# Kernel tuning notes

Measured on AMD Instinct MI355X. Metric: run time of the kernel, lower is better.

The kernel has to match this reference:

```python
import jax, jax.numpy as jnp
import numpy as np

NB_X = 32
NB_Y = 32
EPS = 1e-08


def setup_inputs() -> dict:
    key = jax.random.key(0)
    ks = jax.random.split(key, 10)
    B, L, F, H, D = 16, NB_X * NB_Y + 1, 768, 12, 64
    s = 0.02
    return {
        'x': jax.random.normal(ks[0], (B, L, F), dtype=jnp.float32),
        'wq': jax.random.normal(ks[1], (F, H, D), dtype=jnp.float32) * s,
        'bq': jnp.zeros((H, D), dtype=jnp.float32),
        'wk': jax.random.normal(ks[2], (F, H, D), dtype=jnp.float32) * s,
        'bk': jnp.zeros((H, D), dtype=jnp.float32),
        'wv': jax.random.normal(ks[3], (F, H, D), dtype=jnp.float32) * s,
        'bv': jnp.zeros((H, D), dtype=jnp.float32),
        'wo': jax.random.normal(ks[4], (H, D, F), dtype=jnp.float32) * s,
        'bo': jnp.zeros((F,), dtype=jnp.float32),
        'toeplitz_params': jax.random.normal(ks[5], (H, 4 * NB_X * NB_Y), dtype=jnp.float32),
    }


def _dist_index():
    # relative-position index over the 2D patch grid, flattened to (L0*L0,)
    gi = np.arange(NB_X)
    gj = np.arange(NB_Y)
    idx = ((gi[:, None, None, None] - gi[None, None, :, None] + NB_X) * 2 * NB_Y
           + gj[None, :, None, None] - gj[None, None, None, :] + NB_Y)
    return jnp.asarray(idx.reshape(-1), dtype=jnp.int32)


def reference(x, wq, bq, wk, bk, wv, bv, wo, bo, toeplitz_params):
    H, D = wq.shape[1], wq.shape[2]
    L0 = NB_X * NB_Y  # number of patch tokens (seq len = L0 + 1 with CLS)

    q = jnp.einsum('bqf,fhd->bqhd', x, wq) + bq
    k = jnp.einsum('bkf,fhd->bkhd', x, wk) + bk
    v = jnp.einsum('bkf,fhd->bkhd', x, wv) + bv

    # relu-kernelized scores
    q = jax.nn.relu(q / jnp.sqrt(jnp.float32(D))) + EPS
    k = jax.nn.relu(k) + EPS
    attn = jnp.einsum('bqhd,bkhd->bhqk', q, k)  # [B,H,L,L]

    # per-head Toeplitz relative-position mask via gather
    tm = jnp.take(toeplitz_params, _dist_index(), axis=1).reshape(H, L0, L0)
    tm = jnp.pad(tm, [[0, 0], [1, 0], [0, 0]], constant_values=1.0)
    tm = jnp.pad(tm, [[0, 0], [0, 0], [1, 0]], constant_values=1.0)

    attn = attn * jnp.abs(tm)[None] + EPS
    attn = attn / jnp.sum(attn, axis=-1, keepdims=True)  # sum-normalization

    out = jnp.einsum('bhqk,bkhd->bqhd', attn, v)
    return jnp.einsum('bqhd,hdf->bqf', out, wo) + bo
```

## Files before the change

kernel.cpp:

```cpp
#include <hip/hip_runtime.h>
#include <hip/hip_bf16.h>

#define BB 16
#define LQ 1025
#define FF 768
#define HH 12
#define DD 64
#define EPSF 1e-8f

#define TPSTRIDE 6400
#define QPART_CLS 6270
#define VSTRIDE 1040

typedef unsigned short u16;
typedef __attribute__((ext_vector_type(8))) short  bf16x8;
typedef __attribute__((ext_vector_type(4))) float  f32x4;

__device__ __forceinline__ float bf2f(u16 u) {
    union { unsigned int i; float f; } c;
    c.i = ((unsigned int)u) << 16;
    return c.f;
}

__device__ __forceinline__ u16 f2bf(float f) {
    union { float f; unsigned int i; } c;
    c.f = f;
    unsigned int x = c.i;
    unsigned int r = (x + 0x7fffu + ((x >> 16) & 1u)) >> 16;
    return (u16)r;
}

__global__ __launch_bounds__(256) void convert_x(
    const float* __restrict__ x, u16* __restrict__ xb, int n4)
{
    int i = blockIdx.x * blockDim.x + threadIdx.x;
    const int stride = gridDim.x * blockDim.x;
    for (; i < n4; i += stride) {
        float4 f = ((const float4*)x)[i];
        ushort4 o;
        o.x = f2bf(f.x); o.y = f2bf(f.y); o.z = f2bf(f.z); o.w = f2bf(f.w);
        ((ushort4*)xb)[i] = o;
    }
}

__global__ __launch_bounds__(256) void transpose_w(
    const float* __restrict__ wq, const float* __restrict__ wk,
    const float* __restrict__ wv, const float* __restrict__ wo,
    u16* __restrict__ wqt, u16* __restrict__ wkt,
    u16* __restrict__ wvt, u16* __restrict__ wot)
{
    const int z = blockIdx.z;
    const float* __restrict__ src = (z == 0) ? wq : (z == 1) ? wk : (z == 2) ? wv : wo;
    u16* __restrict__ dst         = (z == 0) ? wqt : (z == 1) ? wkt : (z == 2) ? wvt : wot;

    const int c0 = blockIdx.x * 64;
    const int r0 = blockIdx.y * 64;

    __shared__ u16 tile[64][72];

    const int t   = threadIdx.x;
    const int row = t >> 2;
    const int cs  = (t & 3) << 4;

    {
        const float* p = src + (size_t)(r0 + row) * 768 + c0 + cs;
#pragma unroll
        for (int q = 0; q < 4; ++q) {
            float4 f = *(const float4*)(p + 4 * q);
            ushort4 o;
            o.x = f2bf(f.x); o.y = f2bf(f.y); o.z = f2bf(f.z); o.w = f2bf(f.w);
            *(ushort4*)&tile[row][cs + 4 * q] = o;
        }
    }
    __syncthreads();
    {
        u16* p = dst + (size_t)(c0 + row) * 768 + r0 + cs;
#pragma unroll
        for (int q = 0; q < 4; ++q) {
            ushort4 o;
            o.x = tile[cs + 4 * q + 0][row];
            o.y = tile[cs + 4 * q + 1][row];
            o.z = tile[cs + 4 * q + 2][row];
            o.w = tile[cs + 4 * q + 3][row];
            *(ushort4*)(p + 4 * q) = o;
        }
    }
}

__global__ __launch_bounds__(256) void build_tpa(
    const float* __restrict__ tp, float* __restrict__ tpa)
{
    int i = blockIdx.x * 256 + threadIdx.x;
    if (i >= HH * TPSTRIDE) return;
    int h = i / TPSTRIDE, j = i - h * TPSTRIDE;
    float v;
    if (j < 64) v = 0.f;
    else if (j < 64 + 4096) v = fabsf(tp[h * 4096 + (j - 64)]);
    else v = 1.f;
    tpa[i] = v;
}

__global__ __launch_bounds__(256) void transpose_v(
    const u16* __restrict__ vbuf, u16* __restrict__ vtbuf)
{
    const int bh = blockIdx.y;
    const int lt = blockIdx.x;
    __shared__ u16 tile[64][65];
    const int t   = threadIdx.x;
    const int row = t >> 2;
    const int seg = (t & 3) << 4;

    {
        int l = lt * 64 + row;
        if (l < LQ) {
            const ushort4* p = (const ushort4*)(vbuf + ((size_t)bh * LQ + l) * 64 + seg);
#pragma unroll
            for (int q = 0; q < 4; ++q) {
                ushort4 a = p[q];
                tile[row][seg + 4 * q + 0] = a.x;
                tile[row][seg + 4 * q + 1] = a.y;
                tile[row][seg + 4 * q + 2] = a.z;
                tile[row][seg + 4 * q + 3] = a.w;
            }
        } else {
#pragma unroll
            for (int j = 0; j < 16; ++j) tile[row][seg + j] = 0;
        }
    }
    __syncthreads();
    {
        int kbase = lt * 64 + seg;
        if (kbase + 16 <= VSTRIDE) {
            u16* q = vtbuf + (size_t)bh * 64 * VSTRIDE + (size_t)row * VSTRIDE + kbase;
#pragma unroll
            for (int g = 0; g < 4; ++g) {
                ushort4 o;
                o.x = tile[seg + 4 * g + 0][row];
                o.y = tile[seg + 4 * g + 1][row];
                o.z = tile[seg + 4 * g + 2][row];
                o.w = tile[seg + 4 * g + 3][row];
                *(ushort4*)(q + 4 * g) = o;
            }
        }
    }
}

__global__ __launch_bounds__(256) void gemm_qkv_mfma(
    const u16* __restrict__ xb,
    const u16* __restrict__ wqt, const u16* __restrict__ wkt,
    const u16* __restrict__ wvt,
    const float* __restrict__ bq, const float* __restrict__ bk,
    const float* __restrict__ bv,
    u16* __restrict__ qbuf, u16* __restrict__ kbuf, u16* __restrict__ vbuf)
{
    const int M  = BB * LQ;
    const int m0 = blockIdx.x * 128;
    const int h  = blockIdx.y;
    const int n0 = h * 64;

    __shared__ u16 As[128][40];
    __shared__ u16 Bq[64][40];
    __shared__ u16 Bk[64][40];
    __shared__ u16 Bv[64][40];

    const int t    = threadIdx.x;
    const int wave = t >> 6;
    const int lane = t & 63;
    const int quad = lane >> 4;
    const int l16  = lane & 15;

    const int sm   = t >> 1;
    const int sseg = (t & 1) << 4;
    const int bn   = t >> 2;
    const int bseg = (t & 3) << 3;

    f32x4 acc[3][2][4];
#pragma unroll
    for (int ty = 0; ty < 3; ++ty)
#pragma unroll
        for (int i = 0; i < 2; ++i)
#pragma unroll
            for (int j = 0; j < 4; ++j)
                acc[ty][i][j] = (f32x4){0.f, 0.f, 0.f, 0.f};

    for (int k0 = 0; k0 < 768; k0 += 32) {
        __syncthreads();
        {
            int gm = m0 + sm;
            if (gm < M) {
                const uint4* p = (const uint4*)(xb + (size_t)gm * 768 + k0 + sseg);
                *(uint4*)&As[sm][sseg]     = p[0];
                *(uint4*)&As[sm][sseg + 8] = p[1];
            } else {
                uint4 z; z.x = 0; z.y = 0; z.z = 0; z.w = 0;
                *(uint4*)&As[sm][sseg]     = z;
                *(uint4*)&As[sm][sseg + 8] = z;
            }
        }
        {
            size_t off = (size_t)(n0 + bn) * 768 + k0 + bseg;
            *(uint4*)&Bq[bn][bseg] = *(const uint4*)(wqt + off);
            *(uint4*)&Bk[bn][bseg] = *(const uint4*)(wkt + off);
            *(uint4*)&Bv[bn][bseg] = *(const uint4*)(wvt + off);
        }
        __syncthreads();

        bf16x8 af0 = *(const bf16x8*)&As[(wave << 5) + l16][quad * 8];
        bf16x8 af1 = *(const bf16x8*)&As[(wave << 5) + 16 + l16][quad * 8];
#pragma unroll
        for (int j = 0; j < 4; ++j) {
            bf16x8 bq8 = *(const bf16x8*)&Bq[16 * j + l16][quad * 8];
            acc[0][0][j] = __builtin_amdgcn_mfma_f32_16x16x32_bf16(af0, bq8, acc[0][0][j], 0, 0, 0);
            acc[0][1][j] = __builtin_amdgcn_mfma_f32_16x16x32_bf16(af1, bq8, acc[0][1][j], 0, 0, 0);
            bf16x8 bk8 = *(const bf16x8*)&Bk[16 * j + l16][quad * 8];
            acc[1][0][j] = __builtin_amdgcn_mfma_f32_16x16x32_bf16(af0, bk8, acc[1][0][j], 0, 0, 0);
            acc[1][1][j] = __builtin_amdgcn_mfma_f32_16x16x32_bf16(af1, bk8, acc[1][1][j], 0, 0, 0);
            bf16x8 bv8 = *(const bf16x8*)&Bv[16 * j + l16][quad * 8];
            acc[2][0][j] = __builtin_amdgcn_mfma_f32_16x16x32_bf16(af0, bv8, acc[2][0][j], 0, 0, 0);
            acc[2][1][j] = __builtin_amdgcn_mfma_f32_16x16x32_bf16(af1, bv8, acc[2][1][j], 0, 0, 0);
        }
    }

#pragma unroll
    for (int i = 0; i < 2; ++i) {
#pragma unroll
        for (int reg = 0; reg < 4; ++reg) {
            int gm = m0 + (wave << 5) + (i << 4) + quad * 4 + reg;
            if (gm >= M) continue;
            int b_idx = gm / LQ;
            int l     = gm - b_idx * LQ;
            size_t obase = ((size_t)(b_idx * HH + h) * LQ + l) * 64;
#pragma unroll
            for (int j = 0; j < 4; ++j) {
                int d = 16 * j + l16;
                float vq = acc[0][i][j][reg] + bq[n0 + d];
                vq = fmaxf(vq * 0.125f, 0.f) + EPSF;
                qbuf[obase + d] = f2bf(vq);
                float vk = acc[1][i][j][reg] + bk[n0 + d];
                vk = fmaxf(vk, 0.f) + EPSF;
                kbuf[obase + d] = f2bf(vk);
                float vv = acc[2][i][j][reg] + bv[n0 + d];
                vbuf[obase + d] = f2bf(vv);
            }
        }
    }
}

__global__ __launch_bounds__(256) void attn_fused(
    const u16* __restrict__ qbuf, const u16* __restrict__ kbuf,
    const u16* __restrict__ vtbuf, const float* __restrict__ tpa,
    u16* __restrict__ obuf)
{
    const int bh = blockIdx.y;
    const int b  = bh / HH;
    const int h  = bh - b * HH;
    const int q0 = blockIdx.x * 64;

    __shared__ u16 SQ[64][72];
    __shared__ u16 Ks[64][72];
    __shared__ u16 Vt[64][72];

    const int t    = threadIdx.x;
    const int wave = t >> 6;
    const int lane = t & 63;
    const int quad = lane >> 4;
    const int l16  = lane & 15;
    const int w16  = wave << 4;

    const size_t base  = (size_t)bh * LQ * 64;
    const size_t vbase = (size_t)bh * 64 * VSTRIDE;
    const float* tb = tpa + h * TPSTRIDE;

    const int srow = t >> 2;
    const int sseg = (t & 3) << 4;

    {
        const uint4* qp = (const uint4*)(qbuf + base + (size_t)(q0 + srow) * 64 + sseg);
        *(uint4*)&SQ[srow][sseg]     = qp[0];
        *(uint4*)&SQ[srow][sseg + 8] = qp[1];
    }

    const int qi = q0 + w16 + l16;
    int qpart;
    if (qi == 0) qpart = QPART_CLS;
    else { int qm1 = qi - 1; qpart = (((qm1 >> 5) + 32) << 6) + (qm1 & 31) + 32; }

    int idx[16];
#pragma unroll
    for (int ct = 0; ct < 4; ++ct)
#pragma unroll
        for (int reg = 0; reg < 4; ++reg) {
            int km1 = ct * 16 + quad * 4 + reg - 1;
            idx[ct * 4 + reg] = 64 + qpart - (((km1 >> 5) << 6) + (km1 & 31));
        }

    uint4 kr0, kr1, vr0, vr1;
    {
        uint4 z; z.x = 0; z.y = 0; z.z = 0; z.w = 0;
        int ki = srow;
        if (ki < LQ) {
            const uint4* kp = (const uint4*)(kbuf + base + (size_t)ki * 64 + sseg);
            kr0 = kp[0]; kr1 = kp[1];
        } else { kr0 = z; kr1 = z; }
        const uint4* vp = (const uint4*)(vtbuf + vbase + (size_t)srow * VSTRIDE + sseg);
        vr0 = vp[0]; vr1 = vp[1];
    }

    __syncthreads();

    bf16x8 qf0 = *(const bf16x8*)&SQ[w16 + l16][quad * 8];
    bf16x8 qf1 = *(const bf16x8*)&SQ[w16 + l16][32 + quad * 8];

    f32x4 acc_o[4];
#pragma unroll
    for (int dt = 0; dt < 4; ++dt) acc_o[dt] = (f32x4){0.f, 0.f, 0.f, 0.f};
    float den = 0.f;

    for (int kt = 0; kt < 17; ++kt) {
        __syncthreads();

        *(uint4*)&Ks[srow][sseg]     = kr0;
        *(uint4*)&Ks[srow][sseg + 8] = kr1;
        *(uint4*)&Vt[srow][sseg]     = vr0;
        *(uint4*)&Vt[srow][sseg + 8] = vr1;

        float tmv[16];
#pragma unroll
        for (int e = 0; e < 16; ++e) tmv[e] = tb[idx[e]];

        if (kt < 16) {
            uint4 z; z.x = 0; z.y = 0; z.z = 0; z.w = 0;
            int k0n = (kt + 1) * 64;
            int ki = k0n + srow;
            if (ki < LQ) {
                const uint4* kp = (const uint4*)(kbuf + base + (size_t)ki * 64 + sseg);
                kr0 = kp[0]; kr1 = kp[1];
            } else { kr0 = z; kr1 = z; }
            int vcol = k0n + sseg;
            if (vcol + 16 <= VSTRIDE) {
                const uint4* vp = (const uint4*)(vtbuf + vbase + (size_t)srow * VSTRIDE + vcol);
                vr0 = vp[0]; vr1 = vp[1];
            } else { vr0 = z; vr1 = z; }
        }

        __syncthreads();

        f32x4 acc_s[4];
#pragma unroll
        for (int ct = 0; ct < 4; ++ct) {
            bf16x8 kf0 = *(const bf16x8*)&Ks[ct * 16 + l16][quad * 8];
            bf16x8 kf1 = *(const bf16x8*)&Ks[ct * 16 + l16][32 + quad * 8];
            f32x4 z = (f32x4){0.f, 0.f, 0.f, 0.f};
            z = __builtin_amdgcn_mfma_f32_16x16x32_bf16(kf0, qf0, z, 0, 0, 0);
            z = __builtin_amdgcn_mfma_f32_16x16x32_bf16(kf1, qf1, z, 0, 0, 0);
            acc_s[ct] = z;
        }

        if (kt == 0) { if (quad == 0) tmv[0] = 1.0f; }

#pragma unroll
        for (int ct = 0; ct < 4; ++ct) {
            float s0 = acc_s[ct][0] * tmv[ct * 4 + 0] + EPSF;
            float s1 = acc_s[ct][1] * tmv[ct * 4 + 1] + EPSF;
            float s2 = acc_s[ct][2] * tmv[ct * 4 + 2] + EPSF;
            float s3 = acc_s[ct][3] * tmv[ct * 4 + 3] + EPSF;
            den += (s0 + s1) + (s2 + s3);
            ushort4 w;
            w.x = f2bf(s0); w.y = f2bf(s1); w.z = f2bf(s2); w.w = f2bf(s3);
            *(ushort4*)&SQ[w16 + l16][ct * 16 + quad * 4] = w;
        }
#pragma unroll
        for (int e = 0; e < 16; ++e) idx[e] -= 128;

        __syncthreads();

        {
            bf16x8 a0 = *(const bf16x8*)&SQ[w16 + l16][quad * 8];
            bf16x8 a1 = *(const bf16x8*)&SQ[w16 + l16][32 + quad * 8];
#pragma unroll
            for (int dt = 0; dt < 4; ++dt) {
                bf16x8 b0 = *(const bf16x8*)&Vt[dt * 16 + l16][quad * 8];
                bf16x8 b1 = *(const bf16x8*)&Vt[dt * 16 + l16][32 + quad * 8];
                acc_o[dt] = __builtin_amdgcn_mfma_f32_16x16x32_bf16(a0, b0, acc_o[dt], 0, 0, 0);
                acc_o[dt] = __builtin_amdgcn_mfma_f32_16x16x32_bf16(a1, b1, acc_o[dt], 0, 0, 0);
            }
        }
    }

    den += __shfl_xor(den, 16);
    den += __shfl_xor(den, 32);
    float invd = 1.f / den;

#pragma unroll
    for (int reg = 0; reg < 4; ++reg) {
        int r = quad * 4 + reg;
        float iv = __shfl(invd, r, 64);
        int qrow = q0 + w16 + r;
        if (qrow < LQ) {
            u16* p = obuf + ((size_t)(b * LQ + qrow) * HH + h) * 64;
#pragma unroll
            for (int dt = 0; dt < 4; ++dt)
                p[dt * 16 + l16] = f2bf(acc_o[dt][reg] * iv);
        }
    }
}

__global__ __launch_bounds__(256) void gemm_out_mfma(
    const u16* __restrict__ a, const u16* __restrict__ wot,
    const float* __restrict__ bo, float* __restrict__ out)
{
    const int M  = BB * LQ;
    const int m0 = blockIdx.x * 128;
    const int n0 = blockIdx.y * 64;

    __shared__ u16 As[128][40];
    __shared__ u16 Bs[64][40];

    const int t    = threadIdx.x;
    const int wave = t >> 6;
    const int lane = t & 63;
    const int quad = lane >> 4;
    const int l16  = lane & 15;

    const int sm   = t >> 1;
    const int sseg = (t & 1) << 4;
    const int bn   = t >> 2;
    const int bseg = (t & 3) << 3;

    f32x4 acc[2][4];
#pragma unroll
    for (int i = 0; i < 2; ++i)
#pragma unroll
        for (int j = 0; j < 4; ++j)
            acc[i][j] = (f32x4){0.f, 0.f, 0.f, 0.f};

    for (int k0 = 0; k0 < 768; k0 += 32) {
        __syncthreads();
        {
            int gm = m0 + sm;
            if (gm < M) {
                const uint4* p = (const uint4*)(a + (size_t)gm * 768 + k0 + sseg);
                *(uint4*)&As[sm][sseg]     = p[0];
                *(uint4*)&As[sm][sseg + 8] = p[1];
            } else {
                uint4 z; z.x = 0; z.y = 0; z.z = 0; z.w = 0;
                *(uint4*)&As[sm][sseg]     = z;
                *(uint4*)&As[sm][sseg + 8] = z;
            }
        }
        {
            *(uint4*)&Bs[bn][bseg] =
                *(const uint4*)(wot + (size_t)(n0 + bn) * 768 + k0 + bseg);
        }
        __syncthreads();

        bf16x8 af0 = *(const bf16x8*)&As[(wave << 5) + l16][quad * 8];
        bf16x8 af1 = *(const bf16x8*)&As[(wave << 5) + 16 + l16][quad * 8];
#pragma unroll
        for (int j = 0; j < 4; ++j) {
            bf16x8 b8 = *(const bf16x8*)&Bs[16 * j + l16][quad * 8];
            acc[0][j] = __builtin_amdgcn_mfma_f32_16x16x32_bf16(af0, b8, acc[0][j], 0, 0, 0);
            acc[1][j] = __builtin_amdgcn_mfma_f32_16x16x32_bf16(af1, b8, acc[1][j], 0, 0, 0);
        }
    }

#pragma unroll
    for (int i = 0; i < 2; ++i) {
#pragma unroll
        for (int reg = 0; reg < 4; ++reg) {
            int gm = m0 + (wave << 5) + (i << 4) + quad * 4 + reg;
            if (gm >= M) continue;
            float* p = out + (size_t)gm * 768;
#pragma unroll
            for (int j = 0; j < 4; ++j) {
                int n = n0 + 16 * j + l16;
                p[n] = acc[i][j][reg] + bo[n];
            }
        }
    }
}

extern "C" void kernel_launch(void* const* d_in, const int* in_sizes, int n_in,
                              void* d_out, int out_size, void* d_ws, size_t ws_size,
                              hipStream_t stream) {
    const float* x  = (const float*)d_in[0];
    const float* wq = (const float*)d_in[1];
    const float* bq = (const float*)d_in[2];
    const float* wk = (const float*)d_in[3];
    const float* bk = (const float*)d_in[4];
    const float* wv = (const float*)d_in[5];
    const float* bv = (const float*)d_in[6];
    const float* wo = (const float*)d_in[7];
    const float* bo = (const float*)d_in[8];
    const float* tp = (const float*)d_in[9];
    float* out = (float*)d_out;

    const size_t per = (size_t)BB * HH * LQ * DD;
    const size_t wsz = (size_t)FF * FF;
    u16* ws16  = (u16*)d_ws;
    u16* qbuf  = ws16;
    u16* kbuf  = qbuf + per;
    u16* vbuf  = kbuf + per;
    u16* xb    = vbuf + per;
    u16* wqt   = xb + per;
    u16* wkt   = wqt + wsz;
    u16* wvt   = wkt + wsz;
    u16* wot   = wvt + wsz;
    float* tpa = (float*)(wot + wsz);

    u16* vtbuf = xb;
    u16* obuf  = vbuf;

    convert_x<<<2048, 256, 0, stream>>>(x, xb, (int)(per / 4));
    dim3 gt(12, 12, 4);
    transpose_w<<<gt, 256, 0, stream>>>(wq, wk, wv, wo, wqt, wkt, wvt, wot);
    build_tpa<<<(HH * TPSTRIDE + 255) / 256, 256, 0, stream>>>(tp, tpa);

    dim3 g1(129, 12);
    gemm_qkv_mfma<<<g1, 256, 0, stream>>>(xb, wqt, wkt, wvt, bq, bk, bv,
                                          qbuf, kbuf, vbuf);

    dim3 gv(17, BB * HH);
    transpose_v<<<gv, 256, 0, stream>>>(vbuf, vtbuf);

    dim3 g2(17, BB * HH);
    attn_fused<<<g2, 256, 0, stream>>>(qbuf, kbuf, vtbuf, tpa, obuf);

    dim3 g3(129, 12);
    gemm_out_mfma<<<g3, 256, 0, stream>>>(obuf, wot, bo, out);
}
```

Measured before the change: 484.8 us.

## Use 128x128 wave tiles in both GEMMs and double-buffer K/V in attention

Both projection GEMMs now use a 128x128 block tile with a 2x2 wave layout, giving each wave a 64x64 sub-tile. For the QKV GEMM, the contiguous wqt/wkt/wvt buffers are treated as a single 2304-wide weight matrix, and a new kernel packs the three biases into one array. The attention kernel double-buffers its K and V shared-memory tiles and prefetches two tiles ahead, which cuts the per-iteration barriers from three to one. The intent is more MFMA work per shared-memory load and fewer synchronisations, at the cost of more registers, more LDS and fewer blocks in the grid.

```diff
diff --git a/kernel.cpp b/kernel.cpp
--- a/kernel.cpp
+++ b/kernel.cpp
@@ -100,6 +100,16 @@
     tpa[i] = v;
 }
 
+__global__ __launch_bounds__(256) void pack_bias(
+    const float* __restrict__ bq, const float* __restrict__ bk,
+    const float* __restrict__ bv, float* __restrict__ bias_cat)
+{
+    int i = blockIdx.x * 256 + threadIdx.x;
+    if (i >= 2304) return;
+    float v = (i < 768) ? bq[i] : (i < 1536) ? bk[i - 768] : bv[i - 1536];
+    bias_cat[i] = v;
+}
+
 __global__ __launch_bounds__(256) void transpose_v(
     const u16* __restrict__ vbuf, u16* __restrict__ vtbuf)
 {
@@ -146,42 +156,34 @@
 }
 
 __global__ __launch_bounds__(256) void gemm_qkv_mfma(
-    const u16* __restrict__ xb,
-    const u16* __restrict__ wqt, const u16* __restrict__ wkt,
-    const u16* __restrict__ wvt,
-    const float* __restrict__ bq, const float* __restrict__ bk,
-    const float* __restrict__ bv,
+    const u16* __restrict__ xb, const u16* __restrict__ wt,
+    const float* __restrict__ bias_cat,
     u16* __restrict__ qbuf, u16* __restrict__ kbuf, u16* __restrict__ vbuf)
 {
-    const int M  = BB * LQ;
-    const int m0 = blockIdx.x * 128;
-    const int h  = blockIdx.y;
-    const int n0 = h * 64;
+    const int M   = BB * LQ;
+    const int m0  = blockIdx.x * 128;
+    const int n0g = blockIdx.y * 128;
 
     __shared__ u16 As[128][40];
-    __shared__ u16 Bq[64][40];
-    __shared__ u16 Bk[64][40];
-    __shared__ u16 Bv[64][40];
+    __shared__ u16 Bs[128][40];
 
     const int t    = threadIdx.x;
     const int wave = t >> 6;
     const int lane = t & 63;
     const int quad = lane >> 4;
     const int l16  = lane & 15;
+    const int wm   = (wave >> 1) << 6;
+    const int wn   = (wave & 1) << 6;
 
     const int sm   = t >> 1;
     const int sseg = (t & 1) << 4;
-    const int bn   = t >> 2;
-    const int bseg = (t & 3) << 3;
-
-    f32x4 acc[3][2][4];
-#pragma unroll
-    for (int ty = 0; ty < 3; ++ty)
-#pragma unroll
-        for (int i = 0; i < 2; ++i)
-#pragma unroll
-            for (int j = 0; j < 4; ++j)
-                acc[ty][i][j] = (f32x4){0.f, 0.f, 0.f, 0.f};
+
+    f32x4 acc[4][4];
+#pragma unroll
+    for (int i = 0; i < 4; ++i)
+#pragma unroll
+        for (int j = 0; j < 4; ++j)
+            acc[i][j] = (f32x4){0.f, 0.f, 0.f, 0.f};
 
     for (int k0 = 0; k0 < 768; k0 += 32) {
         __syncthreads();
@@ -198,49 +200,44 @@
             }
         }
         {
-            size_t off = (size_t)(n0 + bn) * 768 + k0 + bseg;
-            *(uint4*)&Bq[bn][bseg] = *(const uint4*)(wqt + off);
-            *(uint4*)&Bk[bn][bseg] = *(const uint4*)(wkt + off);
-            *(uint4*)&Bv[bn][bseg] = *(const uint4*)(wvt + off);
+            const uint4* p = (const uint4*)(wt + (size_t)(n0g + sm) * 768 + k0 + sseg);
+            *(uint4*)&Bs[sm][sseg]     = p[0];
+            *(uint4*)&Bs[sm][sseg + 8] = p[1];
         }
         __syncthreads();
 
-        bf16x8 af0 = *(const bf16x8*)&As[(wave << 5) + l16][quad * 8];
-        bf16x8 af1 = *(const bf16x8*)&As[(wave << 5) + 16 + l16][quad * 8];
-#pragma unroll
-        for (int j = 0; j < 4; ++j) {
-            bf16x8 bq8 = *(const bf16x8*)&Bq[16 * j + l16][quad * 8];
-            acc[0][0][j] = __builtin_amdgcn_mfma_f32_16x16x32_bf16(af0, bq8, acc[0][0][j], 0, 0, 0);
-            acc[0][1][j] = __builtin_amdgcn_mfma_f32_16x16x32_bf16(af1, bq8, acc[0][1][j], 0, 0, 0);
-            bf16x8 bk8 = *(const bf16x8*)&Bk[16 * j + l16][quad * 8];
-            acc[1][0][j] = __builtin_amdgcn_mfma_f32_16x16x32_bf16(af0, bk8, acc[1][0][j], 0, 0, 0);
-            acc[1][1][j] = __builtin_amdgcn_mfma_f32_16x16x32_bf16(af1, bk8, acc[1][1][j], 0, 0, 0);
-            bf16x8 bv8 = *(const bf16x8*)&Bv[16 * j + l16][quad * 8];
-            acc[2][0][j] = __builtin_amdgcn_mfma_f32_16x16x32_bf16(af0, bv8, acc[2][0][j], 0, 0, 0);
-            acc[2][1][j] = __builtin_amdgcn_mfma_f32_16x16x32_bf16(af1, bv8, acc[2][1][j], 0, 0, 0);
-        }
-    }
-
-#pragma unroll
-    for (int i = 0; i < 2; ++i) {
+        bf16x8 af[4], bf[4];
+#pragma unroll
+        for (int i = 0; i < 4; ++i) af[i] = *(const bf16x8*)&As[wm + 16 * i + l16][quad * 8];
+#pragma unroll
+        for (int j = 0; j < 4; ++j) bf[j] = *(const bf16x8*)&Bs[wn + 16 * j + l16][quad * 8];
+#pragma unroll
+        for (int i = 0; i < 4; ++i)
+#pragma unroll
+            for (int j = 0; j < 4; ++j)
+                acc[i][j] = __builtin_amdgcn_mfma_f32_16x16x32_bf16(af[i], bf[j], acc[i][j], 0, 0, 0);
+    }
+
+    const int type = (n0g >= 1536) ? 2 : (n0g >= 768) ? 1 : 0;
+    u16* __restrict__ outb = (type == 0) ? qbuf : (type == 1) ? kbuf : vbuf;
+    const int nbase = n0g - type * 768;
+
+#pragma unroll
+    for (int i = 0; i < 4; ++i) {
 #pragma unroll
         for (int reg = 0; reg < 4; ++reg) {
-            int gm = m0 + (wave << 5) + (i << 4) + quad * 4 + reg;
+            int gm = m0 + wm + 16 * i + quad * 4 + reg;
             if (gm >= M) continue;
             int b_idx = gm / LQ;
             int l     = gm - b_idx * LQ;
-            size_t obase = ((size_t)(b_idx * HH + h) * LQ + l) * 64;
 #pragma unroll
             for (int j = 0; j < 4; ++j) {
-                int d = 16 * j + l16;
-                float vq = acc[0][i][j][reg] + bq[n0 + d];
-                vq = fmaxf(vq * 0.125f, 0.f) + EPSF;
-                qbuf[obase + d] = f2bf(vq);
-                float vk = acc[1][i][j][reg] + bk[n0 + d];
-                vk = fmaxf(vk, 0.f) + EPSF;
-                kbuf[obase + d] = f2bf(vk);
-                float vv = acc[2][i][j][reg] + bv[n0 + d];
-                vbuf[obase + d] = f2bf(vv);
+                int nloc = nbase + wn + 16 * j + l16;
+                int h = nloc >> 6, d = nloc & 63;
+                float v = acc[i][j][reg] + bias_cat[n0g + wn + 16 * j + l16];
+                if (type == 0) v = fmaxf(v * 0.125f, 0.f) + EPSF;
+                else if (type == 1) v = fmaxf(v, 0.f) + EPSF;
+                outb[((size_t)(b_idx * HH + h) * LQ + l) * 64 + d] = f2bf(v);
             }
         }
     }
@@ -257,8 +254,8 @@
     const int q0 = blockIdx.x * 64;
 
     __shared__ u16 SQ[64][72];
-    __shared__ u16 Ks[64][72];
-    __shared__ u16 Vt[64][72];
+    __shared__ u16 Ks[2][64][72];
+    __shared__ u16 Vt[2][64][72];
 
     const int t    = threadIdx.x;
     const int wave = t >> 6;
@@ -311,26 +308,42 @@
     bf16x8 qf0 = *(const bf16x8*)&SQ[w16 + l16][quad * 8];
     bf16x8 qf1 = *(const bf16x8*)&SQ[w16 + l16][32 + quad * 8];
 
+    *(uint4*)&Ks[0][srow][sseg]     = kr0;
+    *(uint4*)&Ks[0][srow][sseg + 8] = kr1;
+    *(uint4*)&Vt[0][srow][sseg]     = vr0;
+    *(uint4*)&Vt[0][srow][sseg + 8] = vr1;
+
+    {
+        uint4 z; z.x = 0; z.y = 0; z.z = 0; z.w = 0;
+        int ki = 64 + srow;
+        if (ki < LQ) {
+            const uint4* kp = (const uint4*)(kbuf + base + (size_t)ki * 64 + sseg);
+            kr0 = kp[0]; kr1 = kp[1];
+        } else { kr0 = z; kr1 = z; }
+        int vcol = 64 + sseg;
+        const uint4* vp = (const uint4*)(vtbuf + vbase + (size_t)srow * VSTRIDE + vcol);
+        vr0 = vp[0]; vr1 = vp[1];
+    }
+
     f32x4 acc_o[4];
 #pragma unroll
     for (int dt = 0; dt < 4; ++dt) acc_o[dt] = (f32x4){0.f, 0.f, 0.f, 0.f};
     float den = 0.f;
 
+    __syncthreads();
+
     for (int kt = 0; kt < 17; ++kt) {
-        __syncthreads();
-
-        *(uint4*)&Ks[srow][sseg]     = kr0;
-        *(uint4*)&Ks[srow][sseg + 8] = kr1;
-        *(uint4*)&Vt[srow][sseg]     = vr0;
-        *(uint4*)&Vt[srow][sseg + 8] = vr1;
-
-        float tmv[16];
-#pragma unroll
-        for (int e = 0; e < 16; ++e) tmv[e] = tb[idx[e]];
+        const int p = kt & 1;
 
         if (kt < 16) {
+            *(uint4*)&Ks[p ^ 1][srow][sseg]     = kr0;
+            *(uint4*)&Ks[p ^ 1][srow][sseg + 8] = kr1;
+            *(uint4*)&Vt[p ^ 1][srow][sseg]     = vr0;
+            *(uint4*)&Vt[p ^ 1][srow][sseg + 8] = vr1;
+        }
+        if (kt < 15) {
             uint4 z; z.x = 0; z.y = 0; z.z = 0; z.w = 0;
-            int k0n = (kt + 1) * 64;
+            int k0n = (kt + 2) * 64;
             int ki = k0n + srow;
             if (ki < LQ) {
                 const uint4* kp = (const uint4*)(kbuf + base + (size_t)ki * 64 + sseg);
@@ -343,13 +356,15 @@
             } else { vr0 = z; vr1 = z; }
         }
 
-        __syncthreads();
+        float tmv[16];
+#pragma unroll
+        for (int e = 0; e < 16; ++e) tmv[e] = tb[idx[e]];
 
         f32x4 acc_s[4];
 #pragma unroll
         for (int ct = 0; ct < 4; ++ct) {
-            bf16x8 kf0 = *(const bf16x8*)&Ks[ct * 16 + l16][quad * 8];
-            bf16x8 kf1 = *(const bf16x8*)&Ks[ct * 16 + l16][32 + quad * 8];
+            bf16x8 kf0 = *(const bf16x8*)&Ks[p][ct * 16 + l16][quad * 8];
+            bf16x8 kf1 = *(const bf16x8*)&Ks[p][ct * 16 + l16][32 + quad * 8];
             f32x4 z = (f32x4){0.f, 0.f, 0.f, 0.f};
             z = __builtin_amdgcn_mfma_f32_16x16x32_bf16(kf0, qf0, z, 0, 0, 0);
             z = __builtin_amdgcn_mfma_f32_16x16x32_bf16(kf1, qf1, z, 0, 0, 0);
@@ -372,19 +387,19 @@
 #pragma unroll
         for (int e = 0; e < 16; ++e) idx[e] -= 128;
 
-        __syncthreads();
-
         {
             bf16x8 a0 = *(const bf16x8*)&SQ[w16 + l16][quad * 8];
             bf16x8 a1 = *(const bf16x8*)&SQ[w16 + l16][32 + quad * 8];
 #pragma unroll
             for (int dt = 0; dt < 4; ++dt) {
-                bf16x8 b0 = *(const bf16x8*)&Vt[dt * 16 + l16][quad * 8];
-                bf16x8 b1 = *(const bf16x8*)&Vt[dt * 16 + l16][32 + quad * 8];
+                bf16x8 b0 = *(const bf16x8*)&Vt[p][dt * 16 + l16][quad * 8];
+                bf16x8 b1 = *(const bf16x8*)&Vt[p][dt * 16 + l16][32 + quad * 8];
                 acc_o[dt] = __builtin_amdgcn_mfma_f32_16x16x32_bf16(a0, b0, acc_o[dt], 0, 0, 0);
                 acc_o[dt] = __builtin_amdgcn_mfma_f32_16x16x32_bf16(a1, b1, acc_o[dt], 0, 0, 0);
             }
         }
+
+        if (kt < 16) __syncthreads();
     }
 
     den += __shfl_xor(den, 16);
@@ -411,25 +426,25 @@
 {
     const int M  = BB * LQ;
     const int m0 = blockIdx.x * 128;
-    const int n0 = blockIdx.y * 64;
+    const int n0 = blockIdx.y * 128;
 
     __shared__ u16 As[128][40];
-    __shared__ u16 Bs[64][40];
+    __shared__ u16 Bs[128][40];
 
     const int t    = threadIdx.x;
     const int wave = t >> 6;
     const int lane = t & 63;
     const int quad = lane >> 4;
     const int l16  = lane & 15;
+    const int wm   = (wave >> 1) << 6;
+    const int wn   = (wave & 1) << 6;
 
     const int sm   = t >> 1;
     const int sseg = (t & 1) << 4;
-    const int bn   = t >> 2;
-    const int bseg = (t & 3) << 3;
-
-    f32x4 acc[2][4];
-#pragma unroll
-    for (int i = 0; i < 2; ++i)
+
+    f32x4 acc[4][4];
+#pragma unroll
+    for (int i = 0; i < 4; ++i)
 #pragma unroll
         for (int j = 0; j < 4; ++j)
             acc[i][j] = (f32x4){0.f, 0.f, 0.f, 0.f};
@@ -449,31 +464,34 @@
             }
         }
         {
-            *(uint4*)&Bs[bn][bseg] =
-                *(const uint4*)(wot + (size_t)(n0 + bn) * 768 + k0 + bseg);
+            const uint4* p = (const uint4*)(wot + (size_t)(n0 + sm) * 768 + k0 + sseg);
+            *(uint4*)&Bs[sm][sseg]     = p[0];
+            *(uint4*)&Bs[sm][sseg + 8] = p[1];
         }
         __syncthreads();
 
-        bf16x8 af0 = *(const bf16x8*)&As[(wave << 5) + l16][quad * 8];
-        bf16x8 af1 = *(const bf16x8*)&As[(wave << 5) + 16 + l16][quad * 8];
-#pragma unroll
-        for (int j = 0; j < 4; ++j) {
-            bf16x8 b8 = *(const bf16x8*)&Bs[16 * j + l16][quad * 8];
-            acc[0][j] = __builtin_amdgcn_mfma_f32_16x16x32_bf16(af0, b8, acc[0][j], 0, 0, 0);
-            acc[1][j] = __builtin_amdgcn_mfma_f32_16x16x32_bf16(af1, b8, acc[1][j], 0, 0, 0);
-        }
-    }
-
-#pragma unroll
-    for (int i = 0; i < 2; ++i) {
+        bf16x8 af[4], bf[4];
+#pragma unroll
+        for (int i = 0; i < 4; ++i) af[i] = *(const bf16x8*)&As[wm + 16 * i + l16][quad * 8];
+#pragma unroll
+        for (int j = 0; j < 4; ++j) bf[j] = *(const bf16x8*)&Bs[wn + 16 * j + l16][quad * 8];
+#pragma unroll
+        for (int i = 0; i < 4; ++i)
+#pragma unroll
+            for (int j = 0; j < 4; ++j)
+                acc[i][j] = __builtin_amdgcn_mfma_f32_16x16x32_bf16(af[i], bf[j], acc[i][j], 0, 0, 0);
+    }
+
+#pragma unroll
+    for (int i = 0; i < 4; ++i) {
 #pragma unroll
         for (int reg = 0; reg < 4; ++reg) {
-            int gm = m0 + (wave << 5) + (i << 4) + quad * 4 + reg;
+            int gm = m0 + wm + 16 * i + quad * 4 + reg;
             if (gm >= M) continue;
             float* p = out + (size_t)gm * 768;
 #pragma unroll
             for (int j = 0; j < 4; ++j) {
-                int n = n0 + 16 * j + l16;
+                int n = n0 + wn + 16 * j + l16;
                 p[n] = acc[i][j][reg] + bo[n];
             }
         }
@@ -507,6 +525,7 @@
     u16* wvt   = wkt + wsz;
     u16* wot   = wvt + wsz;
     float* tpa = (float*)(wot + wsz);
+    float* bias_cat = tpa + HH * TPSTRIDE;
 
     u16* vtbuf = xb;
     u16* obuf  = vbuf;
@@ -515,10 +534,10 @@
     dim3 gt(12, 12, 4);
     transpose_w<<<gt, 256, 0, stream>>>(wq, wk, wv, wo, wqt, wkt, wvt, wot);
     build_tpa<<<(HH * TPSTRIDE + 255) / 256, 256, 0, stream>>>(tp, tpa);
-
-    dim3 g1(129, 12);
-    gemm_qkv_mfma<<<g1, 256, 0, stream>>>(xb, wqt, wkt, wvt, bq, bk, bv,
-                                          qbuf, kbuf, vbuf);
+    pack_bias<<<9, 256, 0, stream>>>(bq, bk, bv, bias_cat);
+
+    dim3 g1(129, 18);
+    gemm_qkv_mfma<<<g1, 256, 0, stream>>>(xb, wqt, bias_cat, qbuf, kbuf, vbuf);
 
     dim3 gv(17, BB * HH);
     transpose_v<<<gv, 256, 0, stream>>>(vbuf, vtbuf);
@@ -526,6 +545,6 @@
     dim3 g2(17, BB * HH);
     attn_fused<<<g2, 256, 0, stream>>>(qbuf, kbuf, vtbuf, tpa, obuf);
 
-    dim3 g3(129, 12);
+    dim3 g3(129, 6);
     gemm_out_mfma<<<g3, 256, 0, stream>>>(obuf, wot, bo, out);
 }
```

After: 481.7 us. About the same (-0.6%).
